# Kernel optimization log

Hardware: AMD Instinct MI355X
Metric: run time of the kernel (lower is better)

The kernel has to match this reference:

```python
import jax, jax.numpy as jnp
import numpy as np
import math

MIN_NORM = 1e-15
EPS = 4e-3  # float32 boundary eps used by PoincareBall.proj
C = 1.0


def artanh(x):
    x = jnp.clip(x, -1.0 + 1e-7, 1.0 - 1e-7)
    return 0.5 * (jnp.log1p(x) - jnp.log1p(-x))


def _norm(x):
    return jnp.maximum(jnp.linalg.norm(x, axis=-1, keepdims=True), MIN_NORM)


def proj(x, c):
    n = _norm(x)
    maxnorm = (1.0 - EPS) / jnp.sqrt(c)
    return jnp.where(n > maxnorm, x / n * maxnorm, x)


def expmap0(u, c):
    sc = jnp.sqrt(c)
    n = _norm(u)
    return jnp.tanh(sc * n) * u / (sc * n)


def logmap0(p, c):
    sc = jnp.sqrt(c)
    n = _norm(p)
    return artanh(sc * n) * p / (sc * n)


def mobius_add(x, y, c):
    x2 = jnp.sum(x * x, -1, keepdims=True)
    y2 = jnp.sum(y * y, -1, keepdims=True)
    xy = jnp.sum(x * y, -1, keepdims=True)
    num = (1 + 2 * c * xy + c * y2) * x + (1 - c * x2) * y
    den = 1 + 2 * c * xy + c * c * x2 * y2
    return num / jnp.maximum(den, MIN_NORM)


def mobius_matvec(m, x, c):
    sc = jnp.sqrt(c)
    xn = _norm(x)
    mx = x @ m.T
    mxn = _norm(mx)
    res = jnp.tanh(mxn / xn * artanh(sc * xn)) * mx / (mxn * sc)
    zero = jnp.all(mx == 0, axis=-1, keepdims=True)
    return jnp.where(zero, jnp.zeros((), x.dtype), res)


def hnn_layer(x, W, b, c):
    # HypLinear (dropout=0, use_bias=1) followed by HypAct(relu); proj_tan0 is identity for PoincareBall.
    res = proj(mobius_matvec(W, x, c), c)
    hb = proj(expmap0(b.reshape(1, -1), c), c)
    res = proj(mobius_add(res, hb, c), c)
    xt = jax.nn.relu(logmap0(res, c))
    return proj(expmap0(xt, c), c)


def setup_inputs():
    key = jax.random.key(0)
    ks = jax.random.split(key, 5)
    B, N, K, D = 4, 2000, 5, 32
    H1, H2 = 160, 32  # H_layer1: 32 -> 32*5, H_layer2: 32 -> 32
    # points on the Poincare ball (small norm so logmap0 is well-conditioned)
    in_feats = 0.05 * jax.random.normal(ks[0], (B, N, D), jnp.float32)
    # one-hot neighbor adjacency [batch, agent, nei, agent]
    nei_idx = jax.random.randint(ks[1], (B, N, K), 0, N)
    in_nei = jax.nn.one_hot(nei_idx, N, dtype=jnp.float32)
    # xavier_uniform with gain sqrt(2), zero bias (reset_parameters)
    b1w = math.sqrt(2.0) * math.sqrt(6.0 / (H1 + D))
    b2w = math.sqrt(2.0) * math.sqrt(6.0 / (H2 + H2))
    W1 = jax.random.uniform(ks[2], (H1, D), jnp.float32, -b1w, b1w)
    W2 = jax.random.uniform(ks[3], (H2, H2), jnp.float32, -b2w, b2w)
    b1 = jnp.zeros((H1,), jnp.float32)
    b2 = jnp.zeros((H2,), jnp.float32)
    return {"in_feats": in_feats, "in_nei": in_nei, "W1": W1, "b1": b1,
            "W2": W2, "b2": b2, "h_dim": 32, "head": 5}


def reference(in_feats, in_nei, W1, b1, W2, b2, h_dim, head):
    c = C
    B, N, D = in_feats.shape
    K = in_nei.shape[2]
    # tangent-space features (proj_tan0 is identity)
    feats = logmap0(in_feats, c)                                   # [B,N,D]
    agent = proj(expmap0(feats[:, :, None, :], c), c)              # [B,N,1,D]
    # one-hot adjacency gather: equals matmul(in_nei, repeat(feats)) in the torch code
    nbr_t = jnp.einsum('bnkm,bmd->bnkd', in_nei, feats)            # [B,N,K,D]
    nbr = proj(expmap0(nbr_t, c), c)
    # query heads
    q = logmap0(hnn_layer(agent, W1, b1, c), c)                    # [B,N,1,h*head]
    q = q.reshape(B, N, 1, h_dim, head).transpose(0, 1, 4, 2, 3)   # [B,N,head,1,h]
    # key heads; the torch code recomputes H_layer1(neighbor_repr) for values with
    # identical weights/inputs (dropout=0), so values == keys and we reuse them.
    kv = logmap0(hnn_layer(nbr, W1, b1, c), c)
    kv = kv.reshape(B, N, K, h_dim, head).transpose(0, 1, 4, 2, 3)  # [B,N,head,K,h]
    att = jax.nn.softmax(jnp.einsum('bnhqd,bnhkd->bnhqk', q, kv), axis=-1)  # [B,N,head,1,K]
    att_record = att.reshape(B, N, head, K)
    out = jnp.einsum('bnhqk,bnhkd->bnhqd', att, kv).mean(axis=2)   # [B,N,1,h]
    out = out.reshape(B, N, h_dim)
    out = proj(expmap0(out, c), c)
    out = hnn_layer(out, W2, b2, c)                                # [B,N,32]
    return out, att_record
```

## Files before the change

### kernel.cpp

```cpp
#include <hip/hip_runtime.h>
#include <math.h>

#define BB 4
#define NN 2000
#define KK 5
#define DD 32
#define H1 160
#define HEAD 5
#define HDIM 32
#define MAXNORM 0.996f
#define MINN 1e-15f

#define TOTAL_BLOCKS 12000

typedef float vfloat4 __attribute__((ext_vector_type(4)));

__device__ __forceinline__ float artanh_f(float x) {
    x = fminf(fmaxf(x, -1.0f + 1e-7f), 1.0f - 1e-7f);
    return 0.5f * (log1pf(x) - log1pf(-x));
}

__device__ __forceinline__ float wave_sum(float v) {
#pragma unroll
    for (int o = 32; o > 0; o >>= 1) v += __shfl_xor(v, o, 64);
    return v;
}

__device__ __forceinline__ float wave_sum32(float v) {
#pragma unroll
    for (int o = 16; o > 0; o >>= 1) v += __shfl_xor(v, o, 64);
    return v;
}

__device__ __forceinline__ void do_find_idx(const float* __restrict__ nei,
                                            int* __restrict__ idx,
                                            int wave, int lane) {
    const float* row = nei + (size_t)wave * NN;
    int pos = -1;
#pragma unroll
    for (int it = 0; it < 8; ++it) {
        int base = it * 256 + lane * 4;
        if (base < NN) {
            vfloat4 v = *(const vfloat4*)(row + base);
            if (v[0] > 0.5f) pos = base;
            if (v[1] > 0.5f) pos = base + 1;
            if (v[2] > 0.5f) pos = base + 2;
            if (v[3] > 0.5f) pos = base + 3;
        }
    }
#pragma unroll
    for (int o = 32; o > 0; o >>= 1) pos = max(pos, __shfl_xor(pos, o, 64));
    if (lane == 0) idx[wave] = pos;
}

__device__ __forceinline__ void do_g(const float* __restrict__ xin,
                                     const float* __restrict__ W1,
                                     const float* __restrict__ b1,
                                     float* __restrict__ g,
                                     int wave, int lane) {
    bool j2ok = lane < (H1 - 128);

    float x = (lane < DD) ? xin[wave * DD + lane] : 0.f;

    float n = fmaxf(sqrtf(wave_sum(x * x)), MINN);
    float fa = artanh_f(n);
    float f = (fa / n) * x;
    float fn = fmaxf(fa, MINN);
    float tp = tanhf(fn);
    float p = (tp / fn) * f;
    float pn = tp;
    if (pn > MAXNORM) p *= MAXNORM / pn;
    float xn = fmaxf(fminf(pn, MAXNORM), MINN);

    float mx0 = 0.f, mx1 = 0.f, mx2 = 0.f;
#pragma unroll
    for (int d = 0; d < DD; ++d) {
        float pd = __shfl(p, d, 64);
        mx0 += W1[lane * DD + d] * pd;
        mx1 += W1[(lane + 64) * DD + d] * pd;
        if (j2ok) mx2 += W1[(lane + 128) * DD + d] * pd;
    }
    float m2 = mx0 * mx0 + mx1 * mx1 + (j2ok ? mx2 * mx2 : 0.f);
    float mxn = fmaxf(sqrtf(wave_sum(m2)), MINN);
    float tr = tanhf(mxn / xn * artanh_f(xn));
    float sc = tr / mxn;
    float r0 = sc * mx0, r1 = sc * mx1, r2 = sc * mx2;
    float rn = tr;
    if (rn > MAXNORM) { float s = MAXNORM / rn; r0 *= s; r1 *= s; r2 *= s; }
    rn = fminf(rn, MAXNORM);

    float bb0 = b1[lane], bb1 = b1[lane + 64], bb2 = j2ok ? b1[lane + 128] : 0.f;
    float bn = fmaxf(sqrtf(wave_sum(bb0 * bb0 + bb1 * bb1 + bb2 * bb2)), MINN);
    float tb = tanhf(bn);
    float bs = tb / bn;
    float h0 = bs * bb0, h1 = bs * bb1, h2 = bs * bb2;
    float hn = tb;
    if (hn > MAXNORM) { float s = MAXNORM / hn; h0 *= s; h1 *= s; h2 *= s; }
    hn = fminf(hn, MAXNORM);

    float x2s = rn * rn;
    float y2s = hn * hn;
    float xys = wave_sum(r0 * h0 + r1 * h1 + (j2ok ? r2 * h2 : 0.f));
    float ca = 1.f + 2.f * xys + y2s;
    float cb = 1.f - x2s;
    float den = fmaxf(1.f + 2.f * xys + x2s * y2s, MINN);
    float a0 = (ca * r0 + cb * h0) / den;
    float a1 = (ca * r1 + cb * h1) / den;
    float a2 = (ca * r2 + cb * h2) / den;
    float an = fmaxf(sqrtf(wave_sum(a0 * a0 + a1 * a1 + (j2ok ? a2 * a2 : 0.f))), MINN);
    if (an > MAXNORM) { float s = MAXNORM / an; a0 *= s; a1 *= s; a2 *= s; }
    float an2 = fmaxf(fminf(an, MAXNORM), MINN);

    float ls = artanh_f(an2) / an2;
    float t0 = fmaxf(ls * a0, 0.f), t1 = fmaxf(ls * a1, 0.f), t2 = fmaxf(ls * a2, 0.f);
    float tn = fmaxf(sqrtf(wave_sum(t0 * t0 + t1 * t1 + (j2ok ? t2 * t2 : 0.f))), MINN);
    float te = tanhf(tn);
    float es = te / tn;
    float y0 = es * t0, y1 = es * t1, y2 = es * t2;
    float yn = te;
    float s2 = (yn > MAXNORM) ? (MAXNORM / yn) : 1.f;
    y0 *= s2; y1 *= s2; y2 *= s2;
    float yn2 = fmaxf(fminf(yn, MAXNORM), MINN);
    float gs = artanh_f(yn2) / yn2;

    float* go = g + (size_t)wave * H1;
    go[lane] = gs * y0;
    go[lane + 64] = gs * y1;
    if (j2ok) go[lane + 128] = gs * y2;
}

__global__ __launch_bounds__(256, 8) void scan_and_g_kernel(const float* __restrict__ nei,
                                                            int* __restrict__ idx,
                                                            const float* __restrict__ xin,
                                                            const float* __restrict__ W1,
                                                            const float* __restrict__ b1,
                                                            float* __restrict__ g) {
    int lane = threadIdx.x & 63;
    int waveInBlock = threadIdx.x >> 6;
    unsigned bi = blockIdx.x;
    unsigned q6 = bi / 6u;
    unsigned r6 = bi - q6 * 6u;
    if (r6 == 5u) {
        int wave = (int)q6 * 4 + waveInBlock;
        do_g(xin, W1, b1, g, wave, lane);
    } else {
        int wave = (int)(q6 * 5u + r6) * 4 + waveInBlock;
        do_find_idx(nei, idx, wave, lane);
    }
}

__global__ __launch_bounds__(256, 4) void fused_att_out_kernel(const float* __restrict__ g,
                                                               const int* __restrict__ idx,
                                                               const float* __restrict__ W2,
                                                               const float* __restrict__ b2,
                                                               float* __restrict__ out,
                                                               float* __restrict__ att_out) {
    int wave = (blockIdx.x * blockDim.x + threadIdx.x) >> 6;
    int lane = threadIdx.x & 63;
    if (wave >= BB * NN) return;
    int r = wave;
    int b = r / NN;
    int d = lane & 31;

    const float* gq = g + (size_t)r * H1;
    float q[HEAD];
#pragma unroll
    for (int h = 0; h < HEAD; ++h) q[h] = gq[d * HEAD + h];

    int nb[KK];
#pragma unroll
    for (int k = 0; k < KK; ++k) nb[k] = idx[r * KK + k];
    float kv[KK][HEAD];
#pragma unroll
    for (int k = 0; k < KK; ++k) {
        const float* gk = g + (size_t)(b * NN + nb[k]) * H1 + d * HEAD;
#pragma unroll
        for (int h = 0; h < HEAD; ++h) kv[k][h] = gk[h];
    }
    float s[KK][HEAD];
#pragma unroll
    for (int k = 0; k < KK; ++k)
#pragma unroll
        for (int h = 0; h < HEAD; ++h) s[k][h] = wave_sum32(q[h] * kv[k][h]);

    float att[HEAD][KK];
#pragma unroll
    for (int h = 0; h < HEAD; ++h) {
        float mxv = s[0][h];
#pragma unroll
        for (int k = 1; k < KK; ++k) mxv = fmaxf(mxv, s[k][h]);
        float sum = 0.f;
#pragma unroll
        for (int k = 0; k < KK; ++k) { att[h][k] = expf(s[k][h] - mxv); sum += att[h][k]; }
        float inv = 1.f / sum;
#pragma unroll
        for (int k = 0; k < KK; ++k) att[h][k] *= inv;
    }
    if (lane < HEAD * KK) {
        int h = lane / KK, k = lane % KK;
        att_out[(size_t)r * HEAD * KK + lane] = att[h][k];
    }

    float o = 0.f;
#pragma unroll
    for (int h = 0; h < HEAD; ++h)
#pragma unroll
        for (int k = 0; k < KK; ++k) o += att[h][k] * kv[k][h];
    o *= (1.f / HEAD);

    float n = fmaxf(sqrtf(wave_sum32(o * o)), MINN);
    float to = tanhf(n);
    o *= to / n;
    float on = to;
    if (on > MAXNORM) o *= MAXNORM / on;
    float xn = fmaxf(fminf(on, MAXNORM), MINN);

    float mx = 0.f;
#pragma unroll
    for (int dd = 0; dd < HDIM; ++dd) {
        float od = __shfl(o, dd, 64);
        mx += W2[d * HDIM + dd] * od;
    }
    float mxn = fmaxf(sqrtf(wave_sum32(mx * mx)), MINN);
    float tr = tanhf(mxn / xn * artanh_f(xn));
    mx *= tr / mxn;
    float rn = tr;
    if (rn > MAXNORM) mx *= MAXNORM / rn;
    rn = fminf(rn, MAXNORM);

    float hb = b2[d];
    float bn = fmaxf(sqrtf(wave_sum32(hb * hb)), MINN);
    float tb = tanhf(bn);
    hb *= tb / bn;
    float hn = tb;
    if (hn > MAXNORM) hb *= MAXNORM / hn;
    hn = fminf(hn, MAXNORM);

    float x2s = rn * rn;
    float y2s = hn * hn;
    float xys = wave_sum32(mx * hb);
    float ca = 1.f + 2.f * xys + y2s;
    float cb = 1.f - x2s;
    float den = fmaxf(1.f + 2.f * xys + x2s * y2s, MINN);
    float a = (ca * mx + cb * hb) / den;
    float an = fmaxf(sqrtf(wave_sum32(a * a)), MINN);
    if (an > MAXNORM) a *= MAXNORM / an;
    float an2 = fmaxf(fminf(an, MAXNORM), MINN);

    a = fmaxf((artanh_f(an2) / an2) * a, 0.f);
    float tn = fmaxf(sqrtf(wave_sum32(a * a)), MINN);
    float te = tanhf(tn);
    a *= te / tn;
    float yn = te;
    if (yn > MAXNORM) a *= MAXNORM / yn;

    if (lane < HDIM) out[(size_t)r * HDIM + lane] = a;
}

extern "C" void kernel_launch(void* const* d_in, const int* in_sizes, int n_in,
                              void* d_out, int out_size, void* d_ws, size_t ws_size,
                              hipStream_t stream) {
    const float* in_feats = (const float*)d_in[0];
    const float* in_nei = (const float*)d_in[1];
    const float* W1 = (const float*)d_in[2];
    const float* b1 = (const float*)d_in[3];
    const float* W2 = (const float*)d_in[4];
    const float* b2 = (const float*)d_in[5];

    int* idx = (int*)d_ws;
    size_t idx_bytes = ((size_t)BB * NN * KK * sizeof(int) + 255) & ~(size_t)255;
    float* g = (float*)((char*)d_ws + idx_bytes);

    float* out = (float*)d_out;
    float* att = out + (size_t)BB * NN * HDIM;

    hipLaunchKernelGGL(scan_and_g_kernel, dim3(TOTAL_BLOCKS), dim3(256), 0, stream,
                       in_nei, idx, in_feats, W1, b1, g);
    hipLaunchKernelGGL(fused_att_out_kernel, dim3((BB * NN * 64 + 255) / 256), dim3(256), 0, stream,
                       g, idx, W2, b2, out, att);
}
```

Before: 623.8 us.

## Scan one-hot adjacency with flat grid-strided float4 loads and direct index writes

Replaces the per-row wave scan of the one-hot adjacency with a flat grid-stride scan. Each thread issues eight independent float4 loads spaced one grid-stride apart, and the one thread that finds the hot element writes the column index directly, with no wave reduction. The g computation now runs in dedicated leading blocks instead of being interleaved with scan blocks. This aims to raise memory-level parallelism on the 320 MB streaming read, at the cost of more registers (launch bounds lowered to 4 waves per SIMD) and of relying on exactly one hot element per row, since rows with none are never written.

```diff
diff --git a/kernel.cpp b/kernel.cpp
--- a/kernel.cpp
+++ b/kernel.cpp
@@ -11,7 +11,12 @@
 #define MAXNORM 0.996f
 #define MINN 1e-15f
 
-#define TOTAL_BLOCKS 12000
+#define NROWS (BB * NN * KK)
+#define NF4   (NROWS * (NN / 4))
+#define F4_PER_ROW (NN / 4)
+#define G_BLOCKS 2000
+#define SCAN_BLOCKS 9766
+#define SCAN_STRIDE (SCAN_BLOCKS * 256)
 
 typedef float vfloat4 __attribute__((ext_vector_type(4)));
 
@@ -32,25 +37,32 @@
     return v;
 }
 
-__device__ __forceinline__ void do_find_idx(const float* __restrict__ nei,
-                                            int* __restrict__ idx,
-                                            int wave, int lane) {
-    const float* row = nei + (size_t)wave * NN;
-    int pos = -1;
-#pragma unroll
-    for (int it = 0; it < 8; ++it) {
-        int base = it * 256 + lane * 4;
-        if (base < NN) {
-            vfloat4 v = *(const vfloat4*)(row + base);
-            if (v[0] > 0.5f) pos = base;
-            if (v[1] > 0.5f) pos = base + 1;
-            if (v[2] > 0.5f) pos = base + 2;
-            if (v[3] > 0.5f) pos = base + 3;
+__device__ __forceinline__ void do_scan(const float* __restrict__ nei,
+                                        int* __restrict__ idx,
+                                        unsigned t) {
+    const vfloat4* __restrict__ p = (const vfloat4*)nei;
+    vfloat4 v[8];
+#pragma unroll
+    for (int j = 0; j < 8; ++j) {
+        unsigned e = t + (unsigned)j * SCAN_STRIDE;
+        if (e < NF4) v[j] = p[e];
+    }
+#pragma unroll
+    for (int j = 0; j < 8; ++j) {
+        unsigned e = t + (unsigned)j * SCAN_STRIDE;
+        if (e < NF4) {
+            int sub = -1;
+            if (v[j][0] > 0.5f) sub = 0;
+            if (v[j][1] > 0.5f) sub = 1;
+            if (v[j][2] > 0.5f) sub = 2;
+            if (v[j][3] > 0.5f) sub = 3;
+            if (sub >= 0) {
+                unsigned row = e / F4_PER_ROW;
+                unsigned col = (e - row * F4_PER_ROW) * 4u + (unsigned)sub;
+                idx[row] = (int)col;
+            }
         }
     }
-#pragma unroll
-    for (int o = 32; o > 0; o >>= 1) pos = max(pos, __shfl_xor(pos, o, 64));
-    if (lane == 0) idx[wave] = pos;
 }
 
 __device__ __forceinline__ void do_g(const float* __restrict__ xin,
@@ -129,24 +141,21 @@
     if (j2ok) go[lane + 128] = gs * y2;
 }
 
-__global__ __launch_bounds__(256, 8) void scan_and_g_kernel(const float* __restrict__ nei,
+__global__ __launch_bounds__(256, 4) void scan_and_g_kernel(const float* __restrict__ nei,
                                                             int* __restrict__ idx,
                                                             const float* __restrict__ xin,
                                                             const float* __restrict__ W1,
                                                             const float* __restrict__ b1,
                                                             float* __restrict__ g) {
-    int lane = threadIdx.x & 63;
-    int waveInBlock = threadIdx.x >> 6;
     unsigned bi = blockIdx.x;
-    unsigned q6 = bi / 6u;
-    unsigned r6 = bi - q6 * 6u;
-    if (r6 == 5u) {
-        int wave = (int)q6 * 4 + waveInBlock;
+    if (bi < G_BLOCKS) {
+        int lane = threadIdx.x & 63;
+        int wave = (int)bi * 4 + (int)(threadIdx.x >> 6);
         do_g(xin, W1, b1, g, wave, lane);
-    } else {
-        int wave = (int)(q6 * 5u + r6) * 4 + waveInBlock;
-        do_find_idx(nei, idx, wave, lane);
-    }
+        return;
+    }
+    unsigned t = (bi - G_BLOCKS) * 256u + threadIdx.x;
+    do_scan(nei, idx, t);
 }
 
 __global__ __launch_bounds__(256, 4) void fused_att_out_kernel(const float* __restrict__ g,
@@ -274,7 +283,7 @@
     float* out = (float*)d_out;
     float* att = out + (size_t)BB * NN * HDIM;
 
-    hipLaunchKernelGGL(scan_and_g_kernel, dim3(TOTAL_BLOCKS), dim3(256), 0, stream,
+    hipLaunchKernelGGL(scan_and_g_kernel, dim3(G_BLOCKS + SCAN_BLOCKS), dim3(256), 0, stream,
                        in_nei, idx, in_feats, W1, b1, g);
     hipLaunchKernelGGL(fused_att_out_kernel, dim3((BB * NN * 64 + 255) / 256), dim3(256), 0, stream,
                        g, idx, W2, b2, out, att);
```

Result: faster. 532.5 us (-14.6%).
